# Kernel tuning notes

Measured on AMD Instinct MI355X. Metric: run time of the kernel, lower is better.

The kernel has to match this reference:

```python
import jax, jax.numpy as jnp
import numpy as np

EMBED_DIM = 1024
NUM_HEADS = 16
HEAD_DIM = EMBED_DIM // NUM_HEADS
SCALE = HEAD_DIM ** -0.5


def setup_inputs() -> dict:
    key = jax.random.key(0)
    ks = jax.random.split(key, 13)
    B, Q, K, E = 2, 1024, 2048, EMBED_DIM
    bound = 1.0 / np.sqrt(E)
    def lin(k1, k2):
        W = jax.random.uniform(k1, (E, E), jnp.float32, -bound, bound)
        b = jax.random.uniform(k2, (E,), jnp.float32, -bound, bound)
        return W, b
    Wq, bq = lin(ks[0], ks[1])
    Wk, bk = lin(ks[2], ks[3])
    Wv, bv = lin(ks[4], ks[5])
    Wo, bo = lin(ks[6], ks[7])
    return {
        "query": jax.random.normal(ks[8], (B, Q, E), jnp.float32),
        "key": jax.random.normal(ks[9], (B, K, E), jnp.float32),
        "value": jax.random.normal(ks[10], (B, K, E), jnp.float32),
        "key_padding_mask": jax.random.randint(ks[11], (B, K), 0, 2).astype(bool),
        "Wq": Wq, "bq": bq, "Wk": Wk, "bk": bk,
        "Wv": Wv, "bv": bv, "Wo": Wo, "bo": bo,
    }


def reference(query, key, value, key_padding_mask, Wq, bq, Wk, bk, Wv, bv, Wo, bo):
    B, Q, E = query.shape
    K = key.shape[1]
    H, D = NUM_HEADS, HEAD_DIM
    # projections (torch Linear: x @ W.T + b)
    q = (query @ Wq.T + bq).reshape(B, Q, H, D).transpose(0, 2, 1, 3)  # [B,H,Q,D]
    k = (key @ Wk.T + bk).reshape(B, K, H, D).transpose(0, 2, 1, 3)    # [B,H,K,D]
    v = (value @ Wv.T + bv).reshape(B, K, H, D).transpose(0, 2, 1, 3)  # [B,H,K,D]
    logits = jnp.einsum('bhqd,bhkd->bhqk', q, k) * SCALE               # [B,H,Q,K]
    logits = jnp.where(key_padding_mask[:, None, None, :], -jnp.inf, logits)
    attn = jax.nn.softmax(logits, axis=-1)
    out = jnp.einsum('bhqk,bhkd->bhqd', attn, v)                        # [B,H,Q,D]
    out = out.transpose(0, 2, 1, 3).reshape(B, Q, E)
    out = out @ Wo.T + bo
    return out
```

## Files before the change

### kernel.cpp

```cpp
#include <hip/hip_runtime.h>

typedef __bf16 bf16_t;
typedef __bf16 bf16x4 __attribute__((ext_vector_type(4)));
typedef __bf16 bf16x8 __attribute__((ext_vector_type(8)));
typedef float f32x4 __attribute__((ext_vector_type(4)));

#define B_ 2
#define H_ 16
#define D_ 64
#define E_ 1024
#define QL 1024
#define KL 2048
#define SCALE_L2E 0.1803368801111204f
#define NEG_BIG -1e30f
#define DEFER_THR 8.0f

__device__ __forceinline__ void gload_lds16(const void* g, void* lds) {
  auto* gp = reinterpret_cast<const __attribute__((address_space(1))) uint32_t*>(
      reinterpret_cast<uintptr_t>(g));
  auto* lp = reinterpret_cast<__attribute__((address_space(3))) uint32_t*>(
      reinterpret_cast<uintptr_t>(lds));
  __builtin_amdgcn_global_load_lds(gp, lp, 16, 0, 0);
}

__global__ __launch_bounds__(256) void cast_all(
    const float* __restrict__ q, const float* __restrict__ k, const float* __restrict__ v,
    const float* __restrict__ wq, const float* __restrict__ wk,
    const float* __restrict__ wv, const float* __restrict__ wo,
    bf16_t* __restrict__ oq, bf16_t* __restrict__ ok, bf16_t* __restrict__ ov,
    bf16_t* __restrict__ owq, bf16_t* __restrict__ owk,
    bf16_t* __restrict__ owv, bf16_t* __restrict__ owo) {
  int blk = blockIdx.x;
  const float* in; bf16_t* out; int base;
  if (blk < 1024)      { in = q;  out = oq;  base = blk; }
  else if (blk < 3072) { in = k;  out = ok;  base = blk - 1024; }
  else if (blk < 5120) { in = v;  out = ov;  base = blk - 3072; }
  else if (blk < 5632) { in = wq; out = owq; base = blk - 5120; }
  else if (blk < 6144) { in = wk; out = owk; base = blk - 5632; }
  else if (blk < 6656) { in = wv; out = owv; base = blk - 6144; }
  else                 { in = wo; out = owo; base = blk - 6656; }
  size_t i = (size_t)base * 256 + threadIdx.x;
  float4 a = ((const float4*)in)[2 * i];
  float4 b = ((const float4*)in)[2 * i + 1];
  bf16x8 o;
  o[0] = (bf16_t)a.x; o[1] = (bf16_t)a.y; o[2] = (bf16_t)a.z; o[3] = (bf16_t)a.w;
  o[4] = (bf16_t)b.x; o[5] = (bf16_t)b.y; o[6] = (bf16_t)b.z; o[7] = (bf16_t)b.w;
  ((bf16x8*)out)[i] = o;
}

__global__ void prep_mask(const unsigned char* __restrict__ mraw, float* __restrict__ bias) {
  __shared__ int flagMis, flagB0;
  int t = threadIdx.x;
  if (t == 0) { flagMis = 0; flagB0 = 0; }
  __syncthreads();
  int a = 0, c = 0;
  for (int i = t; i < B_ * KL; i += 256) {
    if (i & 3) a |= mraw[i]; else c |= mraw[i];
  }
  if (a) atomicOr(&flagMis, 1);
  if (c) atomicOr(&flagB0, 1);
  __syncthreads();
  int mode = (flagMis == 0) ? 0 : (flagB0 ? 1 : 2);
  for (int i = t; i < B_ * KL; i += 256) {
    int mv;
    if (mode == 0)      mv = ((const int*)mraw)[i];
    else if (mode == 1) mv = mraw[i];
    else                mv = (((const float*)mraw)[i] != 0.0f);
    bias[i] = mv ? NEG_BIG : 0.0f;
  }
}

__global__ __launch_bounds__(256, 2)
void qkv_gemm(const bf16_t* __restrict__ Xq, const bf16_t* __restrict__ Xk,
              const bf16_t* __restrict__ Xv, const bf16_t* __restrict__ Wqb,
              const bf16_t* __restrict__ Wkb, const bf16_t* __restrict__ Wvb,
              const float* __restrict__ bq, const float* __restrict__ bk,
              const float* __restrict__ bv,
              bf16_t* __restrict__ qhd, bf16_t* __restrict__ khd, bf16_t* __restrict__ vht) {
  __shared__ alignas(16) bf16_t As[2][128 * 64];
  __shared__ alignas(16) bf16_t Bs[2][128 * 64];
  const int wid = blockIdx.x;
  const int work = (wid & 7) * 80 + (wid >> 3);

  const bf16_t *A, *W;
  const float* bias;
  bf16_t* out;
  int mode, Lshift, row0, col0;
  if (work < 128) {
    A = Xq; W = Wqb; bias = bq; out = qhd; mode = 0; Lshift = 10;
    row0 = (work >> 3) * 128; col0 = (work & 7) * 128;
  } else if (work < 384) {
    int t = work - 128;
    A = Xk; W = Wkb; bias = bk; out = khd; mode = 0; Lshift = 11;
    row0 = (t >> 3) * 128; col0 = (t & 7) * 128;
  } else {
    int t = work - 384;
    A = Wvb; W = Xv; bias = bv; out = vht; mode = 2; Lshift = 0;
    row0 = (t & 7) * 128; col0 = (t >> 3) * 128;
  }

  const int K = 1024;
  const int tid = threadIdx.x;
  const int lane = tid & 63;
  const int w = tid >> 6;
  const int l15 = lane & 15, l4 = lane >> 4;
  const int wr = w >> 1, wc = w & 1;

  f32x4 acc[4][4] = {};

  auto stage = [&](int buf, int kt) {
    const int k0 = kt * 64;
#pragma unroll
    for (int i = 0; i < 4; ++i) {
      int idx = (w * 4 + i) * 64 + lane;
      int r = idx >> 3, c = idx & 7;
      int cs = ((c ^ (r & 7)) * 8);
      gload_lds16(A + (size_t)(row0 + r) * K + k0 + cs, &As[buf][(w * 4 + i) * 512]);
      gload_lds16(W + (size_t)(col0 + r) * K + k0 + cs, &Bs[buf][(w * 4 + i) * 512]);
    }
  };

  auto compute = [&](int buf) {
#pragma unroll
    for (int t = 0; t < 2; ++t) {
      bf16x8 af[4], bfv[4];
#pragma unroll
      for (int i = 0; i < 4; ++i) {
        int r = wr * 64 + i * 16 + l15;
        af[i] = *(const bf16x8*)&As[buf][r * 64 + (((t * 4 + l4) ^ (r & 7)) * 8)];
      }
#pragma unroll
      for (int j = 0; j < 4; ++j) {
        int r = wc * 64 + j * 16 + l15;
        bfv[j] = *(const bf16x8*)&Bs[buf][r * 64 + (((t * 4 + l4) ^ (r & 7)) * 8)];
      }
#pragma unroll
      for (int i = 0; i < 4; ++i)
#pragma unroll
        for (int j = 0; j < 4; ++j)
          acc[i][j] = __builtin_amdgcn_mfma_f32_16x16x32_bf16(af[i], bfv[j], acc[i][j], 0, 0, 0);
    }
  };

  stage(0, 0);
  const int nk = K >> 6;
  for (int kt = 0; kt < nk; ++kt) {
    __syncthreads();
    if (kt + 1 < nk) stage((kt + 1) & 1, kt + 1);
    compute(kt & 1);
  }

#pragma unroll
  for (int i = 0; i < 4; ++i) {
    int mbase = row0 + wr * 64 + i * 16 + l4 * 4;
    f32x4 bvm = {};
    if (mode == 2) bvm = *(const f32x4*)&bias[mbase];
#pragma unroll
    for (int j = 0; j < 4; ++j) {
      int n = col0 + wc * 64 + j * 16 + l15;
      float bv = (mode == 2) ? 0.f : bias[n];
#pragma unroll
      for (int r = 0; r < 4; ++r) {
        float v = acc[i][j][r] + ((mode == 2) ? bvm[r] : bv);
        int m = mbase + r;
        if (mode == 0) {
          int bi = m >> Lshift;
          int ml = m & ((1 << Lshift) - 1);
          size_t dst = ((((size_t)bi * H_ + (n >> 6)) << Lshift) + ml) * D_ + (n & 63);
          out[dst] = (bf16_t)v;
        } else {
          int hh = m >> 6, d = m & 63;
          int bi = n >> 11, kk = n & (KL - 1);
          out[((((size_t)bi * H_ + hh) << 6) + d) * KL + kk] = (bf16_t)v;
        }
      }
    }
  }
}

template <int MODE>
__global__ __launch_bounds__(256, 2)
void gemm_nt(const bf16_t* __restrict__ A, const bf16_t* __restrict__ W,
             const float* __restrict__ bias, void* __restrict__ Cout,
             int M, int N, int K, int Lshift) {
  __shared__ alignas(16) bf16_t As[2][128 * 64];
  __shared__ alignas(16) bf16_t Bs[2][128 * 64];
  const int tid = threadIdx.x;
  const int lane = tid & 63;
  const int w = tid >> 6;
  const int l15 = lane & 15, l4 = lane >> 4;
  const int wr = w >> 1, wc = w & 1;
  const int row0 = blockIdx.x * 128, col0 = blockIdx.y * 128;

  f32x4 acc[4][4] = {};

  auto stage = [&](int buf, int kt) {
    const int k0 = kt * 64;
#pragma unroll
    for (int i = 0; i < 4; ++i) {
      int idx = (w * 4 + i) * 64 + lane;
      int r = idx >> 3, c = idx & 7;
      int cs = ((c ^ (r & 7)) * 8);
      gload_lds16(A + (size_t)(row0 + r) * K + k0 + cs, &As[buf][(w * 4 + i) * 512]);
      gload_lds16(W + (size_t)(col0 + r) * K + k0 + cs, &Bs[buf][(w * 4 + i) * 512]);
    }
  };

  auto compute = [&](int buf) {
#pragma unroll
    for (int t = 0; t < 2; ++t) {
      bf16x8 af[4], bfv[4];
#pragma unroll
      for (int i = 0; i < 4; ++i) {
        int r = wr * 64 + i * 16 + l15;
        af[i] = *(const bf16x8*)&As[buf][r * 64 + (((t * 4 + l4) ^ (r & 7)) * 8)];
      }
#pragma unroll
      for (int j = 0; j < 4; ++j) {
        int r = wc * 64 + j * 16 + l15;
        bfv[j] = *(const bf16x8*)&Bs[buf][r * 64 + (((t * 4 + l4) ^ (r & 7)) * 8)];
      }
#pragma unroll
      for (int i = 0; i < 4; ++i)
#pragma unroll
        for (int j = 0; j < 4; ++j)
          acc[i][j] = __builtin_amdgcn_mfma_f32_16x16x32_bf16(af[i], bfv[j], acc[i][j], 0, 0, 0);
    }
  };

  stage(0, 0);
  const int nk = K >> 6;
  for (int kt = 0; kt < nk; ++kt) {
    __syncthreads();
    if (kt + 1 < nk) stage((kt + 1) & 1, kt + 1);
    compute(kt & 1);
  }

#pragma unroll
  for (int i = 0; i < 4; ++i) {
    int mbase = row0 + wr * 64 + i * 16 + l4 * 4;
#pragma unroll
    for (int j = 0; j < 4; ++j) {
      int n = col0 + wc * 64 + j * 16 + l15;
      float bv = bias[n];
#pragma unroll
      for (int r = 0; r < 4; ++r) {
        float v = acc[i][j][r] + bv;
        int m = mbase + r;
        ((float*)Cout)[(size_t)m * N + n] = v;
      }
    }
  }
}

__global__ __launch_bounds__(128, 2)
void attn_fused(const bf16_t* __restrict__ qh, const bf16_t* __restrict__ kh,
                const bf16_t* __restrict__ vhT, const float* __restrict__ mbias,
                bf16_t* __restrict__ outx) {
  __shared__ alignas(16) bf16_t Ksm[2][64 * 64];
  __shared__ alignas(16) bf16_t Vt[2][64 * 64];
  __shared__ alignas(16) bf16_t Ps[2][16 * 64];

  const int wid = blockIdx.x;
  const int work = (wid & 7) * 128 + (wid >> 3);
  const int qt = work & 31;
  const int bh = work >> 5;
  const int h = bh & 15, b = bh >> 4;

  const int tid = threadIdx.x, lane = tid & 63, w = tid >> 6;
  const int l15 = lane & 15, l4 = lane >> 4;
  const size_t bhs = (size_t)b * H_ + h;

  const bf16_t* qbase = qh + (bhs * QL + qt * 32 + w * 16) * D_;
  bf16x8 qf[2];
#pragma unroll
  for (int t = 0; t < 2; ++t)
    qf[t] = *(const bf16x8*)(qbase + l15 * D_ + t * 32 + l4 * 8);

  float m_run = NEG_BIG, l_run = 0.f;
  f32x4 o_acc[4] = {};

  const bf16_t* kbase = kh + bhs * KL * D_;
  const bf16_t* vtb = vhT + bhs * (size_t)D_ * KL;
  const float* mrow = mbias + (size_t)b * KL;

  auto stage = [&](int bufsel, int kt) {
#pragma unroll
    for (int i = 0; i < 4; ++i) {
      int idx = (w * 4 + i) * 64 + lane;
      int r = idx >> 3, c = idx & 7;
      int cs = (c ^ (r & 7)) * 8;
      gload_lds16(kbase + (size_t)(kt * 64 + r) * D_ + cs, &Ksm[bufsel][idx * 8]);
      gload_lds16(vtb + (size_t)r * KL + kt * 64 + cs, &Vt[bufsel][idx * 8]);
    }
  };

  stage(0, 0);
  __syncthreads();

  for (int kt = 0; kt < KL / 64; ++kt) {
    const int buf = kt & 1;
    if (kt + 1 < KL / 64) stage(buf ^ 1, kt + 1);

    f32x4 mv[4];
#pragma unroll
    for (int ct = 0; ct < 4; ++ct)
      mv[ct] = *(const f32x4*)&mrow[kt * 64 + ct * 16 + l4 * 4];

    f32x4 s[4] = {};
    __builtin_amdgcn_s_setprio(1);
#pragma unroll
    for (int ct = 0; ct < 4; ++ct) {
      int krow = ct * 16 + l15;
#pragma unroll
      for (int t = 0; t < 2; ++t) {
        bf16x8 kf = *(const bf16x8*)&Ksm[buf][krow * 64 + (((t * 4 + l4) ^ (krow & 7)) * 8)];
        s[ct] = __builtin_amdgcn_mfma_f32_16x16x32_bf16(kf, qf[t], s[ct], 0, 0, 0);
      }
    }
    __builtin_amdgcn_s_setprio(0);

    float sv[4][4];
    float mt = NEG_BIG;
#pragma unroll
    for (int ct = 0; ct < 4; ++ct)
#pragma unroll
      for (int r = 0; r < 4; ++r) {
        float x = s[ct][r] * SCALE_L2E + mv[ct][r];
        sv[ct][r] = x;
        mt = fmaxf(mt, x);
      }

    if (!__all(mt <= m_run + DEFER_THR)) {
      mt = fmaxf(mt, __shfl_xor(mt, 16, 64));
      mt = fmaxf(mt, __shfl_xor(mt, 32, 64));
      float mnew = fmaxf(m_run, mt);
      float alpha = exp2f(m_run - mnew);
      m_run = mnew;
      l_run *= alpha;
      float arow[4];
#pragma unroll
      for (int r = 0; r < 4; ++r) arow[r] = __shfl(alpha, l4 * 4 + r, 64);
#pragma unroll
      for (int dt = 0; dt < 4; ++dt)
#pragma unroll
        for (int r = 0; r < 4; ++r) o_acc[dt][r] *= arow[r];
    }

    float rsum = 0.f;
#pragma unroll
    for (int ct = 0; ct < 4; ++ct)
#pragma unroll
      for (int r = 0; r < 4; ++r) {
        float p = exp2f(sv[ct][r] - m_run);
        sv[ct][r] = p;
        rsum += p;
      }
    l_run += rsum;

    char* psrow = (char*)&Ps[w][0] + l15 * 128;
#pragma unroll
    for (int ct = 0; ct < 4; ++ct) {
      bf16x4 pk;
#pragma unroll
      for (int r = 0; r < 4; ++r) pk[r] = (bf16_t)sv[ct][r];
      *(bf16x4*)(psrow + (((ct * 4 + l4) ^ l15) * 8)) = pk;
    }

    __builtin_amdgcn_s_setprio(1);
#pragma unroll
    for (int t = 0; t < 2; ++t) {
      int c0 = t * 8 + l4 * 2;
      bf16x4 plo = *(const bf16x4*)(psrow + ((c0 ^ l15) * 8));
      bf16x4 phi = *(const bf16x4*)(psrow + (((c0 + 1) ^ l15) * 8));
      bf16x8 pa;
#pragma unroll
      for (int j = 0; j < 4; ++j) { pa[j] = plo[j]; pa[j + 4] = phi[j]; }
#pragma unroll
      for (int dt = 0; dt < 4; ++dt) {
        int d = dt * 16 + l15;
        bf16x8 vf = *(const bf16x8*)&Vt[buf][d * 64 + (((t * 4 + l4) ^ (d & 7)) * 8)];
        o_acc[dt] = __builtin_amdgcn_mfma_f32_16x16x32_bf16(pa, vf, o_acc[dt], 0, 0, 0);
      }
    }
    __builtin_amdgcn_s_setprio(0);
    __syncthreads();
  }

  float l_tot = l_run + __shfl_xor(l_run, 16, 64);
  l_tot += __shfl_xor(l_tot, 32, 64);
  float inv = 1.0f / l_tot;
  float irow[4];
#pragma unroll
  for (int r = 0; r < 4; ++r) irow[r] = __shfl(inv, l4 * 4 + r, 64);
#pragma unroll
  for (int r = 0; r < 4; ++r) {
    int qrow = qt * 32 + w * 16 + l4 * 4 + r;
#pragma unroll
    for (int dt = 0; dt < 4; ++dt) {
      int d = dt * 16 + l15;
      outx[((size_t)b * QL + qrow) * E_ + h * D_ + d] = (bf16_t)(o_acc[dt][r] * irow[r]);
    }
  }
}

extern "C" void kernel_launch(void* const* d_in, const int* in_sizes, int n_in,
                              void* d_out, int out_size, void* d_ws, size_t ws_size,
                              hipStream_t stream) {
  const float* query = (const float*)d_in[0];
  const float* key   = (const float*)d_in[1];
  const float* value = (const float*)d_in[2];
  const void*  mask  = d_in[3];
  const float* Wq = (const float*)d_in[4];
  const float* bq = (const float*)d_in[5];
  const float* Wk = (const float*)d_in[6];
  const float* bk = (const float*)d_in[7];
  const float* Wv = (const float*)d_in[8];
  const float* bv = (const float*)d_in[9];
  const float* Wo = (const float*)d_in[10];
  const float* bo = (const float*)d_in[11];

  char* ws = (char*)d_ws;
  bf16_t* Xq  = (bf16_t*)(ws + (0ull  << 20));
  bf16_t* Xk  = (bf16_t*)(ws + (4ull  << 20));
  bf16_t* Xv  = (bf16_t*)(ws + (12ull << 20));
  bf16_t* Wqb = (bf16_t*)(ws + (20ull << 20));
  bf16_t* Wkb = (bf16_t*)(ws + (22ull << 20));
  bf16_t* Wvb = (bf16_t*)(ws + (24ull << 20));
  bf16_t* Wob = (bf16_t*)(ws + (26ull << 20));
  bf16_t* qhd = (bf16_t*)(ws + (28ull << 20));
  bf16_t* khd = (bf16_t*)(ws + (32ull << 20));
  bf16_t* vht = (bf16_t*)(ws + (40ull << 20));
  bf16_t* axo = (bf16_t*)(ws + (48ull << 20));
  float*  mbias = (float*)(ws + (52ull << 20));

  prep_mask<<<1, 256, 0, stream>>>((const unsigned char*)mask, mbias);
  cast_all<<<7168, 256, 0, stream>>>(query, key, value, Wq, Wk, Wv, Wo,
                                     Xq, Xk, Xv, Wqb, Wkb, Wvb, Wob);
  qkv_gemm<<<640, 256, 0, stream>>>(Xq, Xk, Xv, Wqb, Wkb, Wvb, bq, bk, bv,
                                    qhd, khd, vht);
  attn_fused<<<1024, 128, 0, stream>>>(qhd, khd, vht, mbias, axo);
  gemm_nt<1><<<dim3(16, 8), 256, 0, stream>>>(axo, Wob, bo, (float*)d_out,
                                              2048, 1024, 1024, 0);
}
```

Measured before the change: 211.3 us.

## Split attention over key halves with a merge kernel and fold mask prep into cast

The attention kernel now runs 256-thread blocks covering 64 query rows, and each block handles only half of the key sequence (split-K). Each block writes unnormalized fp32 partial outputs plus running max and sum, and a new attn_merge kernel combines the two halves into bf16. The mask preparation runs as an extra block of the cast kernel, which removes one launch. The cost is an extra launch and extra fp32 partial traffic, paid for more parallelism per head and shorter per-block loops.

```diff
diff --git a/kernel.cpp b/kernel.cpp
--- a/kernel.cpp
+++ b/kernel.cpp
@@ -29,8 +29,31 @@
     const float* __restrict__ wv, const float* __restrict__ wo,
     bf16_t* __restrict__ oq, bf16_t* __restrict__ ok, bf16_t* __restrict__ ov,
     bf16_t* __restrict__ owq, bf16_t* __restrict__ owk,
-    bf16_t* __restrict__ owv, bf16_t* __restrict__ owo) {
+    bf16_t* __restrict__ owv, bf16_t* __restrict__ owo,
+    const unsigned char* __restrict__ mraw, float* __restrict__ mbias) {
+  __shared__ int flagMis, flagB0;
   int blk = blockIdx.x;
+  if (blk == 7168) {
+    int t = threadIdx.x;
+    if (t == 0) { flagMis = 0; flagB0 = 0; }
+    __syncthreads();
+    int a = 0, c = 0;
+    for (int i = t; i < B_ * KL; i += 256) {
+      if (i & 3) a |= mraw[i]; else c |= mraw[i];
+    }
+    if (a) atomicOr(&flagMis, 1);
+    if (c) atomicOr(&flagB0, 1);
+    __syncthreads();
+    int mode = (flagMis == 0) ? 0 : (flagB0 ? 1 : 2);
+    for (int i = t; i < B_ * KL; i += 256) {
+      int mv;
+      if (mode == 0)      mv = ((const int*)mraw)[i];
+      else if (mode == 1) mv = mraw[i];
+      else                mv = (((const float*)mraw)[i] != 0.0f);
+      mbias[i] = mv ? NEG_BIG : 0.0f;
+    }
+    return;
+  }
   const float* in; bf16_t* out; int base;
   if (blk < 1024)      { in = q;  out = oq;  base = blk; }
   else if (blk < 3072) { in = k;  out = ok;  base = blk - 1024; }
@@ -48,28 +71,6 @@
   ((bf16x8*)out)[i] = o;
 }
 
-__global__ void prep_mask(const unsigned char* __restrict__ mraw, float* __restrict__ bias) {
-  __shared__ int flagMis, flagB0;
-  int t = threadIdx.x;
-  if (t == 0) { flagMis = 0; flagB0 = 0; }
-  __syncthreads();
-  int a = 0, c = 0;
-  for (int i = t; i < B_ * KL; i += 256) {
-    if (i & 3) a |= mraw[i]; else c |= mraw[i];
-  }
-  if (a) atomicOr(&flagMis, 1);
-  if (c) atomicOr(&flagB0, 1);
-  __syncthreads();
-  int mode = (flagMis == 0) ? 0 : (flagB0 ? 1 : 2);
-  for (int i = t; i < B_ * KL; i += 256) {
-    int mv;
-    if (mode == 0)      mv = ((const int*)mraw)[i];
-    else if (mode == 1) mv = mraw[i];
-    else                mv = (((const float*)mraw)[i] != 0.0f);
-    bias[i] = mv ? NEG_BIG : 0.0f;
-  }
-}
-
 __global__ __launch_bounds__(256, 2)
 void qkv_gemm(const bf16_t* __restrict__ Xq, const bf16_t* __restrict__ Xk,
               const bf16_t* __restrict__ Xv, const bf16_t* __restrict__ Wqb,
@@ -253,25 +254,26 @@
   }
 }
 
-__global__ __launch_bounds__(128, 2)
+__global__ __launch_bounds__(256, 4)
 void attn_fused(const bf16_t* __restrict__ qh, const bf16_t* __restrict__ kh,
                 const bf16_t* __restrict__ vhT, const float* __restrict__ mbias,
-                bf16_t* __restrict__ outx) {
+                float* __restrict__ opart, float* __restrict__ marr,
+                float* __restrict__ larr) {
   __shared__ alignas(16) bf16_t Ksm[2][64 * 64];
   __shared__ alignas(16) bf16_t Vt[2][64 * 64];
-  __shared__ alignas(16) bf16_t Ps[2][16 * 64];
+  __shared__ alignas(16) bf16_t Ps[4][16 * 64];
 
   const int wid = blockIdx.x;
   const int work = (wid & 7) * 128 + (wid >> 3);
-  const int qt = work & 31;
+  const int qt = work & 15;
+  const int half = (work >> 4) & 1;
   const int bh = work >> 5;
   const int h = bh & 15, b = bh >> 4;
 
   const int tid = threadIdx.x, lane = tid & 63, w = tid >> 6;
   const int l15 = lane & 15, l4 = lane >> 4;
-  const size_t bhs = (size_t)b * H_ + h;
-
-  const bf16_t* qbase = qh + (bhs * QL + qt * 32 + w * 16) * D_;
+
+  const bf16_t* qbase = qh + ((size_t)bh * QL + qt * 64 + w * 16) * D_;
   bf16x8 qf[2];
 #pragma unroll
   for (int t = 0; t < 2; ++t)
@@ -280,32 +282,38 @@
   float m_run = NEG_BIG, l_run = 0.f;
   f32x4 o_acc[4] = {};
 
-  const bf16_t* kbase = kh + bhs * KL * D_;
-  const bf16_t* vtb = vhT + bhs * (size_t)D_ * KL;
-  const float* mrow = mbias + (size_t)b * KL;
-
-  auto stage = [&](int bufsel, int kt) {
-#pragma unroll
-    for (int i = 0; i < 4; ++i) {
-      int idx = (w * 4 + i) * 64 + lane;
-      int r = idx >> 3, c = idx & 7;
-      int cs = (c ^ (r & 7)) * 8;
-      gload_lds16(kbase + (size_t)(kt * 64 + r) * D_ + cs, &Ksm[bufsel][idx * 8]);
-      gload_lds16(vtb + (size_t)r * KL + kt * 64 + cs, &Vt[bufsel][idx * 8]);
-    }
+  const bf16_t* kbase = kh + ((size_t)bh * KL + half * (KL / 2)) * D_;
+  const bf16_t* vtb = vhT + (size_t)bh * D_ * KL + half * (KL / 2);
+  const int idx0 = tid, idx1 = tid + 256;
+  const int r0 = idx0 >> 3, cs0 = ((idx0 & 7) ^ (r0 & 7)) * 8;
+  const int r1 = idx1 >> 3, cs1 = ((idx1 & 7) ^ (r1 & 7)) * 8;
+  const bf16_t* kp0 = kbase + r0 * D_ + cs0;
+  const bf16_t* kp1 = kbase + r1 * D_ + cs1;
+  const bf16_t* vp0 = vtb + (size_t)r0 * KL + cs0;
+  const bf16_t* vp1 = vtb + (size_t)r1 * KL + cs1;
+  const float* mptr = mbias + (size_t)b * KL + half * (KL / 2) + l4 * 4;
+
+  auto stage = [&](int bufsel) {
+    gload_lds16(kp0, &Ksm[bufsel][idx0 * 8]);
+    gload_lds16(kp1, &Ksm[bufsel][idx1 * 8]);
+    gload_lds16(vp0, &Vt[bufsel][idx0 * 8]);
+    gload_lds16(vp1, &Vt[bufsel][idx1 * 8]);
+    kp0 += 64 * D_; kp1 += 64 * D_; vp0 += 64; vp1 += 64;
   };
 
-  stage(0, 0);
+  stage(0);
   __syncthreads();
 
-  for (int kt = 0; kt < KL / 64; ++kt) {
+  const int NT = KL / 2 / 64;
+  for (int kt = 0; kt < NT; ++kt) {
     const int buf = kt & 1;
-    if (kt + 1 < KL / 64) stage(buf ^ 1, kt + 1);
+    if (kt + 1 < NT) stage(buf ^ 1);
 
     f32x4 mv[4];
 #pragma unroll
     for (int ct = 0; ct < 4; ++ct)
-      mv[ct] = *(const f32x4*)&mrow[kt * 64 + ct * 16 + l4 * 4];
+      mv[ct] = *(const f32x4*)(mptr + ct * 16);
+    mptr += 64;
 
     f32x4 s[4] = {};
     __builtin_amdgcn_s_setprio(1);
@@ -389,19 +397,49 @@
 
   float l_tot = l_run + __shfl_xor(l_run, 16, 64);
   l_tot += __shfl_xor(l_tot, 32, 64);
-  float inv = 1.0f / l_tot;
-  float irow[4];
-#pragma unroll
-  for (int r = 0; r < 4; ++r) irow[r] = __shfl(inv, l4 * 4 + r, 64);
+
+  const size_t prow = (size_t)(half * 32 + bh) * QL;
 #pragma unroll
   for (int r = 0; r < 4; ++r) {
-    int qrow = qt * 32 + w * 16 + l4 * 4 + r;
+    int qrow = qt * 64 + w * 16 + l4 * 4 + r;
 #pragma unroll
     for (int dt = 0; dt < 4; ++dt) {
       int d = dt * 16 + l15;
-      outx[((size_t)b * QL + qrow) * E_ + h * D_ + d] = (bf16_t)(o_acc[dt][r] * irow[r]);
-    }
-  }
+      opart[(prow + qrow) * D_ + d] = o_acc[dt][r];
+    }
+  }
+  if (l4 == 0) {
+    int q = qt * 64 + w * 16 + l15;
+    marr[prow + q] = m_run;
+    larr[prow + q] = l_tot;
+  }
+}
+
+__global__ __launch_bounds__(256)
+void attn_merge(const float* __restrict__ opart, const float* __restrict__ marr,
+                const float* __restrict__ larr, bf16_t* __restrict__ axo) {
+  int idx = blockIdx.x * 256 + threadIdx.x;
+  int row = idx >> 3;
+  int dseg = (idx & 7) * 8;
+  int bh = row >> 10, q = row & 1023;
+  int b = bh >> 4, h = bh & 15;
+  float m0 = marr[row], m1 = marr[32768 + row];
+  float l0 = larr[row], l1 = larr[32768 + row];
+  float m = fmaxf(m0, m1);
+  float w0 = exp2f(m0 - m), w1 = exp2f(m1 - m);
+  float denom = l0 * w0 + l1 * w1;
+  float s0 = w0 / denom, s1 = w1 / denom;
+  const f32x4* p0 = (const f32x4*)&opart[(size_t)row * 64 + dseg];
+  const f32x4* p1 = (const f32x4*)&opart[(size_t)(32768 + row) * 64 + dseg];
+  f32x4 a0 = p0[0], a1 = p0[1];
+  f32x4 b0 = p1[0], b1 = p1[1];
+  bf16x8 o;
+#pragma unroll
+  for (int i = 0; i < 4; ++i) {
+    o[i]     = (bf16_t)(a0[i] * s0 + b0[i] * s1);
+    o[i + 4] = (bf16_t)(a1[i] * s0 + b1[i] * s1);
+  }
+  *(bf16x8*)&axo[((size_t)b * QL + q) * E_ + h * 64 + dseg] = o;
 }
 
 extern "C" void kernel_launch(void* const* d_in, const int* in_sizes, int n_in,
@@ -433,13 +471,17 @@
   bf16_t* vht = (bf16_t*)(ws + (40ull << 20));
   bf16_t* axo = (bf16_t*)(ws + (48ull << 20));
   float*  mbias = (float*)(ws + (52ull << 20));
-
-  prep_mask<<<1, 256, 0, stream>>>((const unsigned char*)mask, mbias);
-  cast_all<<<7168, 256, 0, stream>>>(query, key, value, Wq, Wk, Wv, Wo,
-                                     Xq, Xk, Xv, Wqb, Wkb, Wvb, Wob);
+  float* opart = (float*)(ws + (0ull << 20));
+  float* marr  = (float*)(ws + (16ull << 20));
+  float* larr  = (float*)(ws + (17ull << 20));
+
+  cast_all<<<7169, 256, 0, stream>>>(query, key, value, Wq, Wk, Wv, Wo,
+                                     Xq, Xk, Xv, Wqb, Wkb, Wvb, Wob,
+                                     (const unsigned char*)mask, mbias);
   qkv_gemm<<<640, 256, 0, stream>>>(Xq, Xk, Xv, Wqb, Wkb, Wvb, bq, bk, bv,
                                     qhd, khd, vht);
-  attn_fused<<<1024, 128, 0, stream>>>(qhd, khd, vht, mbias, axo);
+  attn_fused<<<1024, 256, 0, stream>>>(qhd, khd, vht, mbias, opart, marr, larr);
+  attn_merge<<<1024, 256, 0, stream>>>(opart, marr, larr, axo);
   gemm_nt<1><<<dim3(16, 8), 256, 0, stream>>>(axo, Wob, bo, (float*)d_out,
                                               2048, 1024, 1024, 0);
 }
```

After: 209.6 us. About the same (-0.8%).
